# Kernel tuning notes

Measured on AMD Instinct MI355X. Metric: run time of the kernel, lower is better.

Reference implementation:

```python
import jax, jax.numpy as jnp
import numpy as np

B, N = 16384, 4096
NBLOCKS = 4
BLK = N // NBLOCKS  # 1024


def setup_inputs() -> dict:
    key = jax.random.key(0)
    kx, k1, k2, kb = jax.random.split(key, 4)
    # match torch kaiming-style uniform bounds approximately; exact init values
    # don't affect correctness testing, scale kept modest for stability
    bound_w = float(np.sqrt(3.0) * (np.sqrt(2.0 / (1 + 5)) / np.sqrt(BLK)))
    bound_b = 1.0 / float(np.sqrt(N))
    x = jax.random.normal(kx, (B, N), dtype=jnp.float32)
    w1 = jax.random.uniform(k1, (NBLOCKS, BLK, BLK), jnp.float32, -bound_w, bound_w)
    w2 = jax.random.uniform(k2, (NBLOCKS, BLK, BLK), jnp.float32, -bound_w, bound_w)
    bias = jax.random.uniform(kb, (N,), jnp.float32, -bound_b, bound_b)
    return {"x": x, "w1": w1, "w2": w2, "bias": bias}


def monarch_matmul(x, w1, w2):
    # x: (B, n); w1: (k, q, p) with k*p = n; w2: (l, s, r) with l*r = k*q
    Bd, n = x.shape
    k, q, p = w1.shape
    l, s, r = w2.shape
    # out1[b,k,q] = sum_p x[b,k,p] * w1[k,q,p]
    out1 = jnp.einsum('bkp,kqp->bkq', x.reshape(Bd, k, p), w1)
    # permute (k*q) flat -> (r, l), then transpose to (l, r)
    t = out1.reshape(Bd, r, l).transpose(0, 2, 1)  # (B, l, r)
    # out2[b,l,s] = sum_r t[b,l,r] * w2[l,s,r]
    out2 = jnp.einsum('blr,lsr->bls', t, w2)
    # permute to (B, s, l) then flatten -> (B, s*l)
    return out2.transpose(0, 2, 1).reshape(Bd, s * l)


def reference(x, w1, w2, bias):
    return monarch_matmul(x, w1, w2) + bias
```

## Files before the change

kernel.cpp:

```cpp
#include <hip/hip_runtime.h>
#include <hip/hip_bf16.h>
#include <stdint.h>

typedef __bf16 bf16_t;
typedef bf16_t bf16x8 __attribute__((ext_vector_type(8)));
typedef bf16_t bf16x4 __attribute__((ext_vector_type(4)));
typedef float  f32x4  __attribute__((ext_vector_type(4)));

#define B_DIM 16384

#define BARM()   do { asm volatile("" ::: "memory"); \
                      __builtin_amdgcn_s_barrier();  \
                      asm volatile("" ::: "memory"); } while (0)
#define MEMF()   asm volatile("" ::: "memory")
#define VMCNT6() asm volatile("s_waitcnt vmcnt(6)" ::: "memory")
#define VMCNT0() asm volatile("s_waitcnt vmcnt(0)" ::: "memory")

__device__ __forceinline__ void async_copy16(void* lptr, const void* gptr) {
  __builtin_amdgcn_global_load_lds(
      (const __attribute__((address_space(1))) unsigned int*)gptr,
      (__attribute__((address_space(3))) unsigned int*)lptr, 16, 0, 0);
}

__global__ void cast_all_kernel(const float* __restrict__ x, const float* __restrict__ w1,
                                const float* __restrict__ w2, bf16_t* __restrict__ xb,
                                bf16_t* __restrict__ w1b, bf16_t* __restrict__ w2b) {
  size_t c = (size_t)blockIdx.x * 256 + threadIdx.x;
  const float* s; bf16_t* d; size_t off;
  if (c < 8388608)      { s = x;  d = xb;  off = c; }
  else if (c < 8912896) { s = w1; d = w1b; off = c - 8388608; }
  else                  { s = w2; d = w2b; off = c - 8912896; }
  size_t i = off * 8;
  f32x4 a = *(const f32x4*)(s + i);
  f32x4 b = *(const f32x4*)(s + i + 4);
  bf16x8 o;
  o[0]=(bf16_t)a[0]; o[1]=(bf16_t)a[1]; o[2]=(bf16_t)a[2]; o[3]=(bf16_t)a[3];
  o[4]=(bf16_t)b[0]; o[5]=(bf16_t)b[1]; o[6]=(bf16_t)b[2]; o[7]=(bf16_t)b[3];
  *(bf16x8*)(d + i) = o;
}

template<int EPI>
__global__ __launch_bounds__(512, 2)
void monarch_gemm8(const bf16_t* __restrict__ Ab, const bf16_t* __restrict__ Wb,
                   bf16_t* __restrict__ Outb)
{
  __shared__ __align__(16) char smem[131072];
  const int tid  = threadIdx.x;
  const int lane = tid & 63;
  const int wid  = tid >> 6;
  const int wm   = wid >> 2;
  const int wn   = wid & 3;

  const int pb = blockIdx.x;
  const int lb = (pb & 7) * 128 + (pb >> 3);
  const int zi = lb >> 8;
  const int mt = (lb & 255) >> 2;
  const int nt = lb & 3;

  const size_t brow0 = (size_t)mt * 256;
  const int    ncol0 = nt * 256;

  const bf16_t* Asrc = Ab + brow0 * 4096 + (size_t)zi * 1024;
  const bf16_t* Bsrc = Wb + ((size_t)zi << 20) + (size_t)ncol0 * 1024;

  const int sRow = lane >> 3;
  const int sC   = (lane & 7) ^ sRow;

#define STAGE(BUF, T, H) do {                                                   \
    const bf16_t* _s = (H) < 2 ? Asrc + ((size_t)((H) * 128) * 4096) + (T) * 64 \
                               : Bsrc + ((size_t)(((H)-2) * 128) * 1024) + (T) * 64; \
    const size_t _st = (H) < 2 ? 4096 : 1024;                                   \
    async_copy16(smem + (BUF)*65536 + ((H)>>1)*32768 + ((H)&1)*16384 + wid*1024,\
                 _s + (size_t)(wid * 8 + sRow) * _st + sC * 8);                 \
    async_copy16(smem + (BUF)*65536 + ((H)>>1)*32768 + ((H)&1)*16384 + 8192 + wid*1024, \
                 _s + (size_t)(64 + wid * 8 + sRow) * _st + sC * 8);            \
  } while (0)

  const int cs0 = ((0 + (lane >> 4)) ^ (lane & 7)) * 16;
  const int cs1 = ((4 + (lane >> 4)) ^ (lane & 7)) * 16;
  const int aBase = (wm * 128 + (lane & 15)) * 128;
  const int bBase = 32768 + (wn * 64 + (lane & 15)) * 128;

#define RDA(buf, m, kk) (*(const bf16x8*)(smem + (buf)*65536 + aBase + (m)*2048 + ((kk)?cs1:cs0)))
#define RDB(buf, n, kk) (*(const bf16x8*)(smem + (buf)*65536 + bBase + (n)*2048 + ((kk)?cs1:cs0)))

  f32x4 acc[8][4] = {};
  bf16x8 aM0[4][2], aM1[4][2], bN0[2][2], bN1[2][2];

#define MFMA_QUAD(AR, Aarr, NB, Barr)                                              \
  _Pragma("unroll") for (int m = 0; m < 4; ++m)                                    \
  _Pragma("unroll") for (int n = 0; n < 2; ++n)                                    \
  _Pragma("unroll") for (int kk = 0; kk < 2; ++kk)                                 \
    acc[(AR)+m][(NB)+n] = __builtin_amdgcn_mfma_f32_16x16x32_bf16(                 \
        Aarr[m][kk], Barr[n][kk], acc[(AR)+m][(NB)+n], 0, 0, 0);

#define LD_A0(buf) _Pragma("unroll") for (int m = 0; m < 4; ++m) { \
    aM0[m][0] = RDA(buf,m,0); aM0[m][1] = RDA(buf,m,1); }
#define LD_A1(buf) _Pragma("unroll") for (int m = 0; m < 4; ++m) { \
    aM1[m][0] = RDA(buf,m+4,0); aM1[m][1] = RDA(buf,m+4,1); }
#define LD_B0(buf) _Pragma("unroll") for (int n = 0; n < 2; ++n) { \
    bN0[n][0] = RDB(buf,n,0); bN0[n][1] = RDB(buf,n,1); }
#define LD_B1(buf) _Pragma("unroll") for (int n = 0; n < 2; ++n) { \
    bN1[n][0] = RDB(buf,n+2,0); bN1[n][1] = RDB(buf,n+2,1); }

  STAGE(0,0,0); MEMF(); STAGE(0,0,1); MEMF(); STAGE(0,0,2); MEMF(); STAGE(0,0,3); MEMF();
  STAGE(1,1,0); MEMF(); STAGE(1,1,1); MEMF(); STAGE(1,1,2);
  VMCNT6(); BARM();

  for (int it2 = 0; it2 < 8; ++it2) {
    const int t0 = it2 * 2;
    const bool nl = (it2 < 7);
    LD_A0(0); LD_B0(0); LD_A1(0);
    MEMF(); STAGE(1, t0+1, 3);
    BARM();
    __builtin_amdgcn_s_setprio(1);
    MFMA_QUAD(0, aM0, 0, bN0);
    MFMA_QUAD(4, aM1, 0, bN0);
    __builtin_amdgcn_s_setprio(0);
    LD_B1(0);
    if (nl) { MEMF(); STAGE(0, t0+2, 0); MEMF(); STAGE(0, t0+2, 1);
              MEMF(); STAGE(0, t0+2, 2); VMCNT6(); }
    else    { VMCNT0(); }
    BARM();
    __builtin_amdgcn_s_setprio(1);
    MFMA_QUAD(0, aM0, 2, bN1);
    MFMA_QUAD(4, aM1, 2, bN1);
    __builtin_amdgcn_s_setprio(0);
    LD_A0(1); LD_B0(1); LD_A1(1);
    if (nl) { MEMF(); STAGE(0, t0+2, 3); }
    BARM();
    __builtin_amdgcn_s_setprio(1);
    MFMA_QUAD(0, aM0, 0, bN0);
    MFMA_QUAD(4, aM1, 0, bN0);
    __builtin_amdgcn_s_setprio(0);
    LD_B1(1);
    if (nl) { MEMF(); STAGE(1, t0+3, 0); MEMF(); STAGE(1, t0+3, 1);
              MEMF(); STAGE(1, t0+3, 2); VMCNT6(); }
    BARM();
    __builtin_amdgcn_s_setprio(1);
    MFMA_QUAD(0, aM0, 2, bN1);
    MFMA_QUAD(4, aM1, 2, bN1);
    __builtin_amdgcn_s_setprio(0);
  }

  if (EPI == 0) {
    bf16_t* C0 = (bf16_t*)smem;
    #pragma unroll
    for (int half = 0; half < 2; ++half) {
      BARM();
      if (wm == half) {
        const int rg = lane >> 4, cl = lane & 15;
        const int l = cl & 3, rvb = cl >> 2;
        #pragma unroll
        for (int m = 0; m < 8; ++m)
          #pragma unroll
          for (int n = 0; n < 4; ++n) {
            const int rowb = (m * 16 + rg * 4) * 288 + l * 72 + wn * 16 + n * 4 + rvb;
            #pragma unroll
            for (int j = 0; j < 4; ++j)
              C0[rowb + j * 288] = (bf16_t)acc[m][n][j];
          }
      }
      BARM();
      #pragma unroll
      for (int i = 0; i < 8; ++i) {
        const int s = i * 512 + tid;
        const int row = s >> 5, l2 = (s >> 3) & 3, part = s & 7;
        bf16x8 v = *(const bf16x8*)&C0[row * 288 + l2 * 72 + part * 8];
        *(bf16x8*)&Outb[(brow0 + half * 128 + row) * 4096 +
                        l2 * 1024 + zi * 256 + nt * 64 + part * 8] = v;
      }
    }
  } else {
    bf16_t* C = (bf16_t*)smem;
    #pragma unroll
    for (int half = 0; half < 2; ++half) {
      BARM();
      if (wm == half) {
        const int rg = lane >> 4, cl = lane & 15;
        #pragma unroll
        for (int m = 0; m < 8; ++m)
          #pragma unroll
          for (int n = 0; n < 4; ++n) {
            const int rl = m * 16 + rg * 4;
            const int col = wn * 64 + n * 16 + cl;
            #pragma unroll
            for (int j = 0; j < 4; ++j)
              C[(rl + j) * 264 + col] = (bf16_t)acc[m][n][j];
          }
      }
      BARM();
      #pragma unroll
      for (int i = 0; i < 8; ++i) {
        const int s = i * 512 + tid;
        const int row = s >> 5, ch = s & 31;
        bf16x8 v = *(const bf16x8*)&C[row * 264 + ch * 8];
        *(bf16x8*)&Outb[(brow0 + half * 128 + row) * 4096 +
                        (size_t)zi * 1024 + ncol0 + ch * 8] = v;
      }
    }
  }
#undef RDA
#undef RDB
#undef MFMA_QUAD
#undef LD_A0
#undef LD_A1
#undef LD_B0
#undef LD_B1
#undef STAGE
}

__global__ void permute_bias_kernel(const bf16_t* __restrict__ o2,
                                    const float* __restrict__ bias,
                                    float* __restrict__ out) {
  const int t = blockIdx.x * 256 + threadIdx.x;
  const int b = t >> 7;
  const int s0 = (t & 127) * 8;
  const size_t rowb = (size_t)b * 4096;
  bf16x8 vl[4];
  #pragma unroll
  for (int l = 0; l < 4; ++l) vl[l] = *(const bf16x8*)(o2 + rowb + l * 1024 + s0);
  #pragma unroll
  for (int si = 0; si < 8; ++si) {
    f32x4 bb = *(const f32x4*)(bias + (size_t)(s0 + si) * 4);
    f32x4 o;
    o[0] = (float)vl[0][si] + bb[0];
    o[1] = (float)vl[1][si] + bb[1];
    o[2] = (float)vl[2][si] + bb[2];
    o[3] = (float)vl[3][si] + bb[3];
    *(f32x4*)(out + rowb + (size_t)(s0 + si) * 4) = o;
  }
}

extern "C" void kernel_launch(void* const* d_in, const int* in_sizes, int n_in,
                              void* d_out, int out_size, void* d_ws, size_t ws_size,
                              hipStream_t stream) {
  const float* x    = (const float*)d_in[0];
  const float* w1   = (const float*)d_in[1];
  const float* w2   = (const float*)d_in[2];
  const float* bias = (const float*)d_in[3];
  float* out = (float*)d_out;

  char* ws = (char*)d_ws;
  const size_t xbBytes    = (size_t)B_DIM * 4096 * 2;
  const size_t wBytes     = (size_t)8 << 20;
  bf16_t* xb    = (bf16_t*)(ws);
  bf16_t* w1b   = (bf16_t*)(ws + xbBytes);
  bf16_t* w2b   = (bf16_t*)(ws + xbBytes + wBytes);
  bf16_t* inter = (bf16_t*)(ws + xbBytes + 2 * wBytes);
  bf16_t* o2    = xb;

  cast_all_kernel<<<36864, 256, 0, stream>>>(x, w1, w2, xb, w1b, w2b);
  monarch_gemm8<0><<<1024, 512, 0, stream>>>(xb, w1b, inter);
  monarch_gemm8<1><<<1024, 512, 0, stream>>>(inter, w2b, o2);
  permute_bias_kernel<<<8192, 256, 0, stream>>>(o2, bias, out);
}
```

Before: 461.3 us.

## Fuse fp32-to-bf16 cast of x into first monarch GEMM

```diff
diff --git a/kernel.cpp b/kernel.cpp
--- a/kernel.cpp
+++ b/kernel.cpp
@@ -13,7 +13,9 @@
                       __builtin_amdgcn_s_barrier();  \
                       asm volatile("" ::: "memory"); } while (0)
 #define MEMF()   asm volatile("" ::: "memory")
+#define LGKM0()  asm volatile("s_waitcnt lgkmcnt(0)" ::: "memory")
 #define VMCNT6() asm volatile("s_waitcnt vmcnt(6)" ::: "memory")
+#define VMCNT2() asm volatile("s_waitcnt vmcnt(2)" ::: "memory")
 #define VMCNT0() asm volatile("s_waitcnt vmcnt(0)" ::: "memory")
 
 __device__ __forceinline__ void async_copy16(void* lptr, const void* gptr) {
@@ -22,26 +24,175 @@
       (__attribute__((address_space(3))) unsigned int*)lptr, 16, 0, 0);
 }
 
-__global__ void cast_all_kernel(const float* __restrict__ x, const float* __restrict__ w1,
-                                const float* __restrict__ w2, bf16_t* __restrict__ xb,
-                                bf16_t* __restrict__ w1b, bf16_t* __restrict__ w2b) {
-  size_t c = (size_t)blockIdx.x * 256 + threadIdx.x;
-  const float* s; bf16_t* d; size_t off;
-  if (c < 8388608)      { s = x;  d = xb;  off = c; }
-  else if (c < 8912896) { s = w1; d = w1b; off = c - 8388608; }
-  else                  { s = w2; d = w2b; off = c - 8912896; }
-  size_t i = off * 8;
-  f32x4 a = *(const f32x4*)(s + i);
-  f32x4 b = *(const f32x4*)(s + i + 4);
+__global__ void cast_w_kernel(const float* __restrict__ w1, const float* __restrict__ w2,
+                              bf16_t* __restrict__ w1b, bf16_t* __restrict__ w2b) {
+  const float* src = blockIdx.y ? w2 : w1;
+  bf16_t* dst = blockIdx.y ? w2b : w1b;
+  size_t i = ((size_t)blockIdx.x * 256 + threadIdx.x) * 8;
+  f32x4 a = *(const f32x4*)(src + i);
+  f32x4 b = *(const f32x4*)(src + i + 4);
   bf16x8 o;
   o[0]=(bf16_t)a[0]; o[1]=(bf16_t)a[1]; o[2]=(bf16_t)a[2]; o[3]=(bf16_t)a[3];
   o[4]=(bf16_t)b[0]; o[5]=(bf16_t)b[1]; o[6]=(bf16_t)b[2]; o[7]=(bf16_t)b[3];
-  *(bf16x8*)(d + i) = o;
-}
-
-template<int EPI>
+  *(bf16x8*)(dst + i) = o;
+}
+
 __global__ __launch_bounds__(512, 2)
-void monarch_gemm8(const bf16_t* __restrict__ Ab, const bf16_t* __restrict__ Wb,
+void monarch_gemm1f(const float* __restrict__ Xf, const bf16_t* __restrict__ Wb,
+                    bf16_t* __restrict__ Outb)
+{
+  __shared__ __align__(16) char smem[131072];
+  const int tid  = threadIdx.x;
+  const int lane = tid & 63;
+  const int wid  = tid >> 6;
+  const int wm   = wid >> 2;
+  const int wn   = wid & 3;
+
+  const int pb = blockIdx.x;
+  const int lb = (pb & 7) * 128 + (pb >> 3);
+  const int zi = lb >> 8;
+  const int mt = (lb & 255) >> 2;
+  const int nt = lb & 3;
+
+  const size_t brow0 = (size_t)mt * 256;
+  const int    ncol0 = nt * 256;
+
+  const float*  Axf  = Xf + brow0 * 4096 + (size_t)zi * 1024;
+  const bf16_t* Bsrc = Wb + ((size_t)zi << 20) + (size_t)ncol0 * 1024;
+
+  const int sRow = lane >> 3;
+  const int sC   = (lane & 7) ^ sRow;
+
+#define STAGEB(BUF, T, H) do {                                                  \
+    const bf16_t* _s = Bsrc + ((size_t)(((H)-2) * 128) * 1024) + (T) * 64;      \
+    async_copy16(smem + (BUF)*65536 + 32768 + ((H)&1)*16384 + wid*1024,         \
+                 _s + (size_t)(wid * 8 + sRow) * 1024 + sC * 8);                \
+    async_copy16(smem + (BUF)*65536 + 32768 + ((H)&1)*16384 + 8192 + wid*1024,  \
+                 _s + (size_t)(64 + wid * 8 + sRow) * 1024 + sC * 8);           \
+  } while (0)
+
+  const int ar = (tid >> 3) * 4;
+  const int ac = tid & 7;
+  f32x4 aw[8];
+#define ALOADX(T) do { MEMF();                                                  \
+    _Pragma("unroll") for (int q = 0; q < 4; ++q) {                             \
+      const float* _p = Axf + (size_t)(ar + q) * 4096 + (T) * 64 + ac * 8;      \
+      aw[2*q] = *(const f32x4*)_p; aw[2*q+1] = *(const f32x4*)(_p + 4); }       \
+    MEMF(); } while (0)
+#define ACVTX(BUF) do { MEMF();                                                 \
+    _Pragma("unroll") for (int q = 0; q < 4; ++q) {                             \
+      f32x4 _u = aw[2*q], _v = aw[2*q+1]; bf16x8 _pk;                           \
+      _pk[0]=(bf16_t)_u[0]; _pk[1]=(bf16_t)_u[1]; _pk[2]=(bf16_t)_u[2];         \
+      _pk[3]=(bf16_t)_u[3]; _pk[4]=(bf16_t)_v[0]; _pk[5]=(bf16_t)_v[1];         \
+      _pk[6]=(bf16_t)_v[2]; _pk[7]=(bf16_t)_v[3];                               \
+      const int _r = ar + q;                                                    \
+      *(bf16x8*)(smem + (BUF)*65536 + _r * 128 + ((ac ^ (_r & 7)) * 16)) = _pk; } \
+    MEMF(); } while (0)
+
+  const int cs0 = ((0 + (lane >> 4)) ^ (lane & 7)) * 16;
+  const int cs1 = ((4 + (lane >> 4)) ^ (lane & 7)) * 16;
+  const int aBase = (wm * 128 + (lane & 15)) * 128;
+  const int bBase = 32768 + (wn * 64 + (lane & 15)) * 128;
+
+#define RDA(buf, m, kk) (*(const bf16x8*)(smem + (buf)*65536 + aBase + (m)*2048 + ((kk)?cs1:cs0)))
+#define RDB(buf, n, kk) (*(const bf16x8*)(smem + (buf)*65536 + bBase + (n)*2048 + ((kk)?cs1:cs0)))
+
+  f32x4 acc[8][4] = {};
+  bf16x8 aM0[4][2], aM1[4][2], bN0[2][2], bN1[2][2];
+
+#define MFMA_M(AR, Aarr)                                                           \
+  __builtin_amdgcn_s_setprio(1);                                                   \
+  _Pragma("unroll") for (int m = 0; m < 4; ++m)                                    \
+  _Pragma("unroll") for (int n = 0; n < 2; ++n)                                    \
+  _Pragma("unroll") for (int kk = 0; kk < 2; ++kk) {                               \
+    acc[(AR)+m][n]   = __builtin_amdgcn_mfma_f32_16x16x32_bf16(                    \
+        Aarr[m][kk], bN0[n][kk], acc[(AR)+m][n], 0, 0, 0);                         \
+    acc[(AR)+m][2+n] = __builtin_amdgcn_mfma_f32_16x16x32_bf16(                    \
+        Aarr[m][kk], bN1[n][kk], acc[(AR)+m][2+n], 0, 0, 0);                       \
+  }                                                                                \
+  __builtin_amdgcn_s_setprio(0);
+
+#define LD_A0(buf) _Pragma("unroll") for (int m = 0; m < 4; ++m) { \
+    aM0[m][0] = RDA(buf,m,0); aM0[m][1] = RDA(buf,m,1); }
+#define LD_A1(buf) _Pragma("unroll") for (int m = 0; m < 4; ++m) { \
+    aM1[m][0] = RDA(buf,m+4,0); aM1[m][1] = RDA(buf,m+4,1); }
+#define LD_B0(buf) _Pragma("unroll") for (int n = 0; n < 2; ++n) { \
+    bN0[n][0] = RDB(buf,n,0); bN0[n][1] = RDB(buf,n,1); }
+#define LD_B1(buf) _Pragma("unroll") for (int n = 0; n < 2; ++n) { \
+    bN1[n][0] = RDB(buf,n+2,0); bN1[n][1] = RDB(buf,n+2,1); }
+
+  ALOADX(0); ACVTX(0);
+  STAGEB(0,0,2); MEMF(); STAGEB(0,0,3); MEMF();
+  STAGEB(1,1,2);
+  VMCNT2(); LGKM0(); BARM();
+
+  for (int it2 = 0; it2 < 8; ++it2) {
+    const int t0 = it2 * 2;
+    const bool nl = (it2 < 7);
+    ALOADX(t0+1);
+    LD_A0(0); LD_B0(0); LD_B1(0);
+    ACVTX(1);
+    MEMF(); STAGEB(1, t0+1, 3);
+    LGKM0();
+    BARM();
+    MFMA_M(0, aM0);
+    LD_A1(0);
+    if (nl) { MEMF(); STAGEB(0, t0+2, 2); VMCNT2(); }
+    else    { VMCNT0(); }
+    BARM();
+    MFMA_M(4, aM1);
+    if (nl) ALOADX(t0+2);
+    LD_A0(1); LD_B0(1); LD_B1(1);
+    if (nl) { ACVTX(0); MEMF(); STAGEB(0, t0+2, 3); LGKM0(); }
+    BARM();
+    MFMA_M(0, aM0);
+    LD_A1(1);
+    if (nl) { MEMF(); STAGEB(1, t0+3, 2); VMCNT2(); }
+    BARM();
+    MFMA_M(4, aM1);
+  }
+
+  bf16_t* C0 = (bf16_t*)smem;
+  #pragma unroll
+  for (int half = 0; half < 2; ++half) {
+    BARM();
+    if (wm == half) {
+      const int rg = lane >> 4, cl = lane & 15;
+      const int l = cl & 3, rvb = cl >> 2;
+      #pragma unroll
+      for (int m = 0; m < 8; ++m)
+        #pragma unroll
+        for (int n = 0; n < 4; ++n) {
+          const int rowb = (m * 16 + rg * 4) * 288 + l * 72 + wn * 16 + n * 4 + rvb;
+          #pragma unroll
+          for (int j = 0; j < 4; ++j)
+            C0[rowb + j * 288] = (bf16_t)acc[m][n][j];
+        }
+    }
+    BARM();
+    #pragma unroll
+    for (int i = 0; i < 8; ++i) {
+      const int s = i * 512 + tid;
+      const int row = s >> 5, l2 = (s >> 3) & 3, part = s & 7;
+      bf16x8 v = *(const bf16x8*)&C0[row * 288 + l2 * 72 + part * 8];
+      *(bf16x8*)&Outb[(brow0 + half * 128 + row) * 4096 +
+                      l2 * 1024 + zi * 256 + nt * 64 + part * 8] = v;
+    }
+  }
+#undef RDA
+#undef RDB
+#undef MFMA_M
+#undef LD_A0
+#undef LD_A1
+#undef LD_B0
+#undef LD_B1
+#undef STAGEB
+#undef ALOADX
+#undef ACVTX
+}
+
+__global__ __launch_bounds__(512, 2)
+void monarch_gemm2(const bf16_t* __restrict__ Ab, const bf16_t* __restrict__ Wb,
                    bf16_t* __restrict__ Outb)
 {
   __shared__ __align__(16) char smem[131072];
@@ -143,61 +294,31 @@
     __builtin_amdgcn_s_setprio(0);
   }
 
-  if (EPI == 0) {
-    bf16_t* C0 = (bf16_t*)smem;
+  bf16_t* C = (bf16_t*)smem;
+  #pragma unroll
+  for (int half = 0; half < 2; ++half) {
+    BARM();
+    if (wm == half) {
+      const int rg = lane >> 4, cl = lane & 15;
+      #pragma unroll
+      for (int m = 0; m < 8; ++m)
+        #pragma unroll
+        for (int n = 0; n < 4; ++n) {
+          const int rl = m * 16 + rg * 4;
+          const int col = wn * 64 + n * 16 + cl;
+          #pragma unroll
+          for (int j = 0; j < 4; ++j)
+            C[(rl + j) * 264 + col] = (bf16_t)acc[m][n][j];
+        }
+    }
+    BARM();
     #pragma unroll
-    for (int half = 0; half < 2; ++half) {
-      BARM();
-      if (wm == half) {
-        const int rg = lane >> 4, cl = lane & 15;
-        const int l = cl & 3, rvb = cl >> 2;
-        #pragma unroll
-        for (int m = 0; m < 8; ++m)
-          #pragma unroll
-          for (int n = 0; n < 4; ++n) {
-            const int rowb = (m * 16 + rg * 4) * 288 + l * 72 + wn * 16 + n * 4 + rvb;
-            #pragma unroll
-            for (int j = 0; j < 4; ++j)
-              C0[rowb + j * 288] = (bf16_t)acc[m][n][j];
-          }
-      }
-      BARM();
-      #pragma unroll
-      for (int i = 0; i < 8; ++i) {
-        const int s = i * 512 + tid;
-        const int row = s >> 5, l2 = (s >> 3) & 3, part = s & 7;
-        bf16x8 v = *(const bf16x8*)&C0[row * 288 + l2 * 72 + part * 8];
-        *(bf16x8*)&Outb[(brow0 + half * 128 + row) * 4096 +
-                        l2 * 1024 + zi * 256 + nt * 64 + part * 8] = v;
-      }
-    }
-  } else {
-    bf16_t* C = (bf16_t*)smem;
-    #pragma unroll
-    for (int half = 0; half < 2; ++half) {
-      BARM();
-      if (wm == half) {
-        const int rg = lane >> 4, cl = lane & 15;
-        #pragma unroll
-        for (int m = 0; m < 8; ++m)
-          #pragma unroll
-          for (int n = 0; n < 4; ++n) {
-            const int rl = m * 16 + rg * 4;
-            const int col = wn * 64 + n * 16 + cl;
-            #pragma unroll
-            for (int j = 0; j < 4; ++j)
-              C[(rl + j) * 264 + col] = (bf16_t)acc[m][n][j];
-          }
-      }
-      BARM();
-      #pragma unroll
-      for (int i = 0; i < 8; ++i) {
-        const int s = i * 512 + tid;
-        const int row = s >> 5, ch = s & 31;
-        bf16x8 v = *(const bf16x8*)&C[row * 264 + ch * 8];
-        *(bf16x8*)&Outb[(brow0 + half * 128 + row) * 4096 +
-                        (size_t)zi * 1024 + ncol0 + ch * 8] = v;
-      }
+    for (int i = 0; i < 8; ++i) {
+      const int s = i * 512 + tid;
+      const int row = s >> 5, ch = s & 31;
+      bf16x8 v = *(const bf16x8*)&C[row * 264 + ch * 8];
+      *(bf16x8*)&Outb[(brow0 + half * 128 + row) * 4096 +
+                      (size_t)zi * 1024 + ncol0 + ch * 8] = v;
     }
   }
 #undef RDA
@@ -242,16 +363,15 @@
   float* out = (float*)d_out;
 
   char* ws = (char*)d_ws;
-  const size_t xbBytes    = (size_t)B_DIM * 4096 * 2;
   const size_t wBytes     = (size_t)8 << 20;
-  bf16_t* xb    = (bf16_t*)(ws);
-  bf16_t* w1b   = (bf16_t*)(ws + xbBytes);
-  bf16_t* w2b   = (bf16_t*)(ws + xbBytes + wBytes);
-  bf16_t* inter = (bf16_t*)(ws + xbBytes + 2 * wBytes);
-  bf16_t* o2    = xb;
-
-  cast_all_kernel<<<36864, 256, 0, stream>>>(x, w1, w2, xb, w1b, w2b);
-  monarch_gemm8<0><<<1024, 512, 0, stream>>>(xb, w1b, inter);
-  monarch_gemm8<1><<<1024, 512, 0, stream>>>(inter, w2b, o2);
+  const size_t interBytes = (size_t)B_DIM * 4096 * 2;
+  bf16_t* w1b   = (bf16_t*)(ws);
+  bf16_t* w2b   = (bf16_t*)(ws + wBytes);
+  bf16_t* inter = (bf16_t*)(ws + 2 * wBytes);
+  bf16_t* o2    = (bf16_t*)(ws + 2 * wBytes + interBytes);
+
+  cast_w_kernel<<<dim3(2048, 2), 256, 0, stream>>>(w1, w2, w1b, w2b);
+  monarch_gemm1f<<<1024, 512, 0, stream>>>(x, w1b, inter);
+  monarch_gemm2<<<1024, 512, 0, stream>>>(inter, w2b, o2);
   permute_bias_kernel<<<8192, 256, 0, stream>>>(o2, bias, out);
 }
```

Measured after the change: 484.9 us. 5.1% more time.
